# Kernel optimization log

Hardware: AMD Instinct MI355X
Metric: run time of the kernel (lower is better)

## Reference

```python
import jax, jax.numpy as jnp
import numpy as np


def setup_inputs() -> dict:
    key = jax.random.key(0)
    T, B, D, H = 512, 64, 512, 512
    k0, k1, k2, k3 = jax.random.split(key, 4)
    x = jax.random.normal(k0, (T, B, D), dtype=jnp.float32)
    # packed-sequence lengths, descending (as PackedSequence requires), at least T//2
    lengths = jnp.sort(jax.random.randint(k1, (B,), T // 2, T + 1))[::-1].astype(jnp.int64)
    s = 1.0 / np.sqrt(H)
    # gates stacked in order (i, f, c, o): same math as 8 separate per-gate linears
    Wx = jax.random.normal(k2, (4 * H, D), dtype=jnp.float32) * s
    Wh = jax.random.normal(k3, (4 * H, H), dtype=jnp.float32) * s
    # reset_parameters(): b_i = b_c = b_o = 0, b_f = 1
    b = jnp.concatenate([jnp.zeros(H), jnp.ones(H), jnp.zeros(2 * H)]).astype(jnp.float32)
    return {"x": x, "lengths": lengths, "Wx": Wx, "Wh": Wh, "b": b}


def reference(x, lengths, Wx, Wh, b):
    T, B, D = x.shape
    H = Wh.shape[1]
    # input projections for all timesteps at once (one big GEMM)
    xg = jnp.einsum('tbd,gd->tbg', x, Wx) + b  # [T, B, 4H]
    # validity mask per (t, b): packed recurrence only updates active rows
    mask = (jnp.arange(T)[:, None] < lengths[None, :])[..., None]  # [T, B, 1]

    def step(carry, inp):
        h, c = carry
        xg_t, m = inp
        g = xg_t + h @ Wh.T  # [B, 4H]
        i, f, cc, o = jnp.split(g, 4, axis=-1)
        i = jax.nn.sigmoid(i)
        f = jax.nn.sigmoid(f)
        o = jax.nn.sigmoid(o)
        c_t = f * c + i * jnp.tanh(cc)
        h_t = o * jnp.tanh(c_t)
        c_new = jnp.where(m, c_t, c)
        h_new = jnp.where(m, h_t, h)
        out_t = jnp.where(m, h_new, jnp.zeros((), x.dtype))
        return (h_new, c_new), out_t

    h0 = jnp.zeros((B, H), dtype=x.dtype)
    (h_T, c_T), out = jax.lax.scan(step, (h0, h0), (xg, mask))
    return out  # padded equivalent of the PackedSequence output, [T, B, H]
```

## Files before the change

kernel.cpp:

```cpp
#include <hip/hip_runtime.h>
#include <stdint.h>


#define TT 512
#define BB 64
#define DD 512
#define HH 512
#define NWG 256
#define NTHR 512
#define GR 8

typedef short short8 __attribute__((ext_vector_type(8)));
typedef float f32x4 __attribute__((ext_vector_type(4)));

__device__ __forceinline__ uint16_t bf16_rne(float f) {
  uint32_t u = __float_as_uint(f);
  u += 0x7fffu + ((u >> 16) & 1u);
  return (uint16_t)(u >> 16);
}

__device__ __forceinline__ void split2(float f, uint16_t &hi, uint16_t &lo) {
  uint16_t h = bf16_rne(f);
  hi = h;
  lo = bf16_rne(f - __uint_as_float(((uint32_t)h) << 16));
}

__device__ __forceinline__ float sigf(float v) { return 1.0f / (1.0f + __expf(-v)); }
__device__ __forceinline__ float tanh_(float v) {
  return 1.0f - 2.0f / (__expf(2.0f * v) + 1.0f);
}

__global__ void build_frags(const float* __restrict__ W, uint32_t* __restrict__ frag) {
  const int tid = blockIdx.x * 256 + threadIdx.x;
  const int lane = tid & 63;
  const int ks = (tid >> 6) & 15;
  const int nblk = tid >> 10;
  const int col = nblk * 16 + (lane & 15);
  const int k0 = ks * 32 + ((lane >> 4) << 3);
  const float* src = W + (size_t)col * 512 + k0;
  float4 a = *(const float4*)(src);
  float4 b = *(const float4*)(src + 4);
  float v[8] = {a.x, a.y, a.z, a.w, b.x, b.y, b.z, b.w};
  uint32_t hw[4], lw[4];
#pragma unroll
  for (int j = 0; j < 4; ++j) {
    uint16_t h0, l0, h1, l1;
    split2(v[2 * j], h0, l0);
    split2(v[2 * j + 1], h1, l1);
    hw[j] = (uint32_t)h0 | ((uint32_t)h1 << 16);
    lw[j] = (uint32_t)l0 | ((uint32_t)l1 << 16);
  }
  uint4* dst = (uint4*)(frag + (size_t)tid * 8);
  dst[0] = make_uint4(hw[0], hw[1], hw[2], hw[3]);
  dst[1] = make_uint4(lw[0], lw[1], lw[2], lw[3]);
}

__global__ __launch_bounds__(NTHR, 2) void lstm_main(
    const float* __restrict__ x, const int* __restrict__ len,
    const float* __restrict__ bias, const uint32_t* __restrict__ fragWx,
    const uint32_t* __restrict__ fragWh, uint32_t* __restrict__ h_pair,
    float* __restrict__ out) {
  const int tid = threadIdx.x;
  const int lane = tid & 63;
  const int wave = tid >> 6;
  const int gp = wave >> 1;
  const int kh = wave & 1;
  const int group = blockIdx.x & 7;
  const int jblk = blockIdx.x >> 3;
  const int b0 = group * GR;
  const int j0 = jblk << 4;
  uint32_t* hbase = h_pair + (size_t)group * 2 * (GR * HH);

  __shared__ uint16_t AH[GR * 512];
  __shared__ uint16_t AL[GR * 512];
  __shared__ float ex[8][GR][16];
  __shared__ float c_st[GR][16];
  __shared__ float h_st[GR][16];
  __shared__ float bias_l[4][16];
  __shared__ int len_l[GR];

  if (tid < GR * 16) {
    c_st[tid >> 4][tid & 15] = 0.0f;
    h_st[tid >> 4][tid & 15] = 0.0f;
  }
  if (tid < 64) bias_l[tid >> 4][tid & 15] = bias[(size_t)(tid >> 4) * HH + j0 + (tid & 15)];
  if (tid < GR) len_l[tid] = len[b0 + tid];

  short8 bxh[8], bxl[8], bhh[8], bhl[8];
  {
    const int nblk = gp * 32 + jblk;
#pragma unroll
    for (int ksl = 0; ksl < 8; ++ksl) {
      const size_t idx = ((size_t)(nblk * 16 + kh * 8 + ksl) * 64 + lane) * 8;
      uint4 vh = *(const uint4*)(fragWx + idx);
      uint4 vl = *(const uint4*)(fragWx + idx + 4);
      bxh[ksl] = __builtin_bit_cast(short8, vh);
      bxl[ksl] = __builtin_bit_cast(short8, vl);
      uint4 wh = *(const uint4*)(fragWh + idx);
      uint4 wl = *(const uint4*)(fragWh + idx + 4);
      bhh[ksl] = __builtin_bit_cast(short8, wh);
      bhl[ksl] = __builtin_bit_cast(short8, wl);
    }
  }

  const int arow = lane & 7;
  const int achk = (lane >> 4) << 4;
  const int axr = arow << 4;
  const char* rowH = (const char*)AH + arow * 1024;
  const char* rowL = (const char*)AL + arow * 1024;

  f32x4 hh = {0.f, 0.f, 0.f, 0.f}, lh = {0.f, 0.f, 0.f, 0.f}, hl = {0.f, 0.f, 0.f, 0.f};
  float4 xp[2];

#define LOAD_XP(tt)                                                            \
  _Pragma("unroll") for (int i = 0; i < 2; ++i) {                              \
    const int flat4 = i * 2048 + tid * 4;                                      \
    const int row = flat4 >> 9;                                                \
    const int col = flat4 & 511;                                               \
    xp[i] = *(const float4*)(x + ((size_t)(tt) * BB + b0 + row) * DD + col);   \
  }

#define STAGE_XP()                                                             \
  _Pragma("unroll") for (int i = 0; i < 2; ++i) {                              \
    const int flat4 = i * 2048 + tid * 4;                                      \
    const int row = flat4 >> 9;                                                \
    const int col = flat4 & 511;                                               \
    uint16_t h0, l0, h1, l1, h2, l2, h3, l3;                                   \
    split2(xp[i].x, h0, l0);                                                   \
    split2(xp[i].y, h1, l1);                                                   \
    split2(xp[i].z, h2, l2);                                                   \
    split2(xp[i].w, h3, l3);                                                   \
    const uint32_t hw0 = (uint32_t)h0 | ((uint32_t)h1 << 16);                  \
    const uint32_t hw1 = (uint32_t)h2 | ((uint32_t)h3 << 16);                  \
    const uint32_t lw0 = (uint32_t)l0 | ((uint32_t)l1 << 16);                  \
    const uint32_t lw1 = (uint32_t)l2 | ((uint32_t)l3 << 16);                  \
    const int off = row * 1024 + ((col * 2) ^ (row << 4));                     \
    *(uint2*)((char*)AH + off) = make_uint2(hw0, hw1);                         \
    *(uint2*)((char*)AL + off) = make_uint2(lw0, lw1);                         \
  }

#define X_MFMA()                                                               \
  hh = (f32x4){0.f, 0.f, 0.f, 0.f};                                           \
  lh = (f32x4){0.f, 0.f, 0.f, 0.f};                                           \
  hl = (f32x4){0.f, 0.f, 0.f, 0.f};                                           \
  _Pragma("unroll") for (int ksl = 0; ksl < 8; ++ksl) {                        \
    const int off = ((kh * 8 + ksl) * 64 + achk) ^ axr;                        \
    short8 ah = *(const short8*)(rowH + off);                                  \
    short8 al = *(const short8*)(rowL + off);                                  \
    hh = __builtin_amdgcn_mfma_f32_16x16x32_bf16(ah, bxh[ksl], hh, 0, 0, 0);   \
    lh = __builtin_amdgcn_mfma_f32_16x16x32_bf16(al, bxh[ksl], lh, 0, 0, 0);   \
    hl = __builtin_amdgcn_mfma_f32_16x16x32_bf16(ah, bxl[ksl], hl, 0, 0, 0);   \
  }

  LOAD_XP(0);
  __syncthreads();
  STAGE_XP();
  __syncthreads();
  X_MFMA();
  LOAD_XP(1);

  for (int t = 0; t < TT; ++t) {
    const int rbuf = t & 1;
    const int wbuf = rbuf ^ 1;

    if (t > 0) {
      const uint32_t tagp = (((uint32_t)(t - 1)) >> 1) & 3u;
      const uint32_t EXd = ((tagp & 1u) << 14) | ((tagp >> 1) << 30);
      const uint64_t EX2 = ((uint64_t)EXd << 32) | EXd;
      const uint64_t MK2 = 0x4000400040004000ull;
      const unsigned long long* pb =
          (const unsigned long long*)(hbase + (size_t)rbuf * (GR * HH)) +
          (size_t)tid * 4;
      uint64_t w0, w1, w2, w3;
      for (;;) {
        w0 = __hip_atomic_load(pb + 0, __ATOMIC_RELAXED, __HIP_MEMORY_SCOPE_AGENT);
        w1 = __hip_atomic_load(pb + 1, __ATOMIC_RELAXED, __HIP_MEMORY_SCOPE_AGENT);
        w2 = __hip_atomic_load(pb + 2, __ATOMIC_RELAXED, __HIP_MEMORY_SCOPE_AGENT);
        w3 = __hip_atomic_load(pb + 3, __ATOMIC_RELAXED, __HIP_MEMORY_SCOPE_AGENT);
        const uint64_t bad =
            (((w0 ^ EX2) | (w1 ^ EX2) | (w2 ^ EX2) | (w3 ^ EX2)) & MK2);
        if (bad == 0ull) break;
      }
      __syncthreads();

      {
        const uint32_t CM = ~0x40004000u;
        uint32_t d0 = (uint32_t)w0 & CM, d1 = (uint32_t)(w0 >> 32) & CM;
        uint32_t d2 = (uint32_t)w1 & CM, d3 = (uint32_t)(w1 >> 32) & CM;
        uint32_t d4 = (uint32_t)w2 & CM, d5 = (uint32_t)(w2 >> 32) & CM;
        uint32_t d6 = (uint32_t)w3 & CM, d7 = (uint32_t)(w3 >> 32) & CM;
        const uint32_t hi0 = (d0 & 0xFFFFu) | (d1 << 16);
        const uint32_t lo0 = (d0 >> 16) | (d1 & 0xFFFF0000u);
        const uint32_t hi1 = (d2 & 0xFFFFu) | (d3 << 16);
        const uint32_t lo1 = (d2 >> 16) | (d3 & 0xFFFF0000u);
        const uint32_t hi2 = (d4 & 0xFFFFu) | (d5 << 16);
        const uint32_t lo2 = (d4 >> 16) | (d5 & 0xFFFF0000u);
        const uint32_t hi3 = (d6 & 0xFFFFu) | (d7 << 16);
        const uint32_t lo3 = (d6 >> 16) | (d7 & 0xFFFF0000u);
        const int woff = wave * 1024 + ((lane * 16) ^ (wave << 4));
        *(uint4*)((char*)AH + woff) = make_uint4(hi0, hi1, hi2, hi3);
        *(uint4*)((char*)AL + woff) = make_uint4(lo0, lo1, lo2, lo3);
      }
      __syncthreads();

#pragma unroll
      for (int ksl = 0; ksl < 8; ++ksl) {
        const int off = ((kh * 8 + ksl) * 64 + achk) ^ axr;
        short8 ah = *(const short8*)(rowH + off);
        short8 al = *(const short8*)(rowL + off);
        hh = __builtin_amdgcn_mfma_f32_16x16x32_bf16(ah, bhh[ksl], hh, 0, 0, 0);
        lh = __builtin_amdgcn_mfma_f32_16x16x32_bf16(al, bhh[ksl], lh, 0, 0, 0);
        hl = __builtin_amdgcn_mfma_f32_16x16x32_bf16(ah, bhl[ksl], hl, 0, 0, 0);
      }
    }

    {
      const int crow = (lane >> 4) << 2;
      const int ccol = lane & 15;
      if (crow < GR) {
#pragma unroll
        for (int r = 0; r < 4; ++r) ex[wave][crow + r][ccol] = hh[r] + lh[r] + hl[r];
      }
    }
    __syncthreads();

    if (tid < GR * 16) {
      const int brow = tid >> 4;
      const int jc = tid & 15;
      const float p0 = ex[0][brow][jc] + ex[1][brow][jc] + bias_l[0][jc];
      const float p1 = ex[2][brow][jc] + ex[3][brow][jc] + bias_l[1][jc];
      const float p2 = ex[4][brow][jc] + ex[5][brow][jc] + bias_l[2][jc];
      const float p3 = ex[6][brow][jc] + ex[7][brow][jc] + bias_l[3][jc];
      const float ig = sigf(p0);
      const float fg = sigf(p1);
      const float cc = tanh_(p2);
      const float og = sigf(p3);
      const float co = c_st[brow][jc];
      const float ct = fg * co + ig * cc;
      const float ht = og * tanh_(ct);
      const bool m = (t < len_l[brow]);
      const float cn = m ? ct : co;
      const float hn = m ? ht : h_st[brow][jc];
      c_st[brow][jc] = cn;
      h_st[brow][jc] = hn;
      out[((size_t)t * BB + b0 + brow) * HH + j0 + jc] = m ? ht : 0.0f;
      uint16_t ph, pl;
      split2(hn, ph, pl);
      const uint32_t tagw = (((uint32_t)t) >> 1) & 3u;
      const uint32_t TB = ((tagw & 1u) << 14) | ((tagw >> 1) << 30);
      const uint32_t hv = ((uint32_t)ph | ((uint32_t)pl << 16)) | TB;
      __hip_atomic_store(hbase + (size_t)wbuf * (GR * HH) + brow * HH + j0 + jc,
                         hv, __ATOMIC_RELAXED, __HIP_MEMORY_SCOPE_AGENT);
    }

    if (t + 1 < TT) {
      STAGE_XP();
      __syncthreads();
      X_MFMA();
      LOAD_XP(min(t + 2, TT - 1));
    }
  }
}

extern "C" void kernel_launch(void* const* d_in, const int* in_sizes, int n_in,
                              void* d_out, int out_size, void* d_ws, size_t ws_size,
                              hipStream_t stream) {
  const float* x = (const float*)d_in[0];
  const int* len = (const int*)d_in[1];
  const float* Wx = (const float*)d_in[2];
  const float* Wh = (const float*)d_in[3];
  const float* bias = (const float*)d_in[4];
  float* out = (float*)d_out;

  const size_t FRAG_DW = (size_t)128 * 16 * 64 * 8;
  uint32_t* fragWx = (uint32_t*)d_ws;
  uint32_t* fragWh = fragWx + FRAG_DW;
  uint32_t* h_pair = fragWh + FRAG_DW;

  hipMemsetAsync(h_pair, 0xFF, (size_t)8 * 2 * GR * HH * 4, stream);

  build_frags<<<dim3(512), dim3(256), 0, stream>>>(Wx, fragWx);
  build_frags<<<dim3(512), dim3(256), 0, stream>>>(Wh, fragWh);

  void* args[] = {(void*)&x,      (void*)&len,    (void*)&bias, (void*)&fragWx,
                  (void*)&fragWh, (void*)&h_pair, (void*)&out};
  hipLaunchCooperativeKernel((void*)lstm_main, dim3(NWG), dim3(NTHR), args, 0, stream);
}
```

Baseline: 1.445 ms.

## Halve workgroups by doubling batch rows per group in the LSTM recurrence

Changes the work split from 8 batch groups of 8 rows to 4 groups of 16 rows, so 128 workgroups each fill the full 16-row MFMA tile instead of wasting half of it. Each thread now polls and unpacks 8 tagged h words, spinning on the first word before reading the rest, and the shared-memory swizzle is adjusted for 16 rows. Fewer workgroups take part in each step's cross-workgroup exchange, but each does twice the gate math and handles twice the x staging per step, which may lengthen the per-step critical path.

```diff
diff --git a/kernel.cpp b/kernel.cpp
--- a/kernel.cpp
+++ b/kernel.cpp
@@ -6,9 +6,9 @@
 #define BB 64
 #define DD 512
 #define HH 512
-#define NWG 256
+#define NWG 128
 #define NTHR 512
-#define GR 8
+#define GR 16
 
 typedef short short8 __attribute__((ext_vector_type(8)));
 typedef float f32x4 __attribute__((ext_vector_type(4)));
@@ -55,7 +55,7 @@
   dst[1] = make_uint4(lw[0], lw[1], lw[2], lw[3]);
 }
 
-__global__ __launch_bounds__(NTHR, 2) void lstm_main(
+__global__ __launch_bounds__(NTHR, 2) void lstm5(
     const float* __restrict__ x, const int* __restrict__ len,
     const float* __restrict__ bias, const uint32_t* __restrict__ fragWx,
     const uint32_t* __restrict__ fragWh, uint32_t* __restrict__ h_pair,
@@ -65,8 +65,8 @@
   const int wave = tid >> 6;
   const int gp = wave >> 1;
   const int kh = wave & 1;
-  const int group = blockIdx.x & 7;
-  const int jblk = blockIdx.x >> 3;
+  const int group = blockIdx.x & 3;
+  const int jblk = blockIdx.x >> 2;
   const int b0 = group * GR;
   const int j0 = jblk << 4;
   uint32_t* hbase = h_pair + (size_t)group * 2 * (GR * HH);
@@ -92,28 +92,27 @@
 #pragma unroll
     for (int ksl = 0; ksl < 8; ++ksl) {
       const size_t idx = ((size_t)(nblk * 16 + kh * 8 + ksl) * 64 + lane) * 8;
-      uint4 vh = *(const uint4*)(fragWx + idx);
-      uint4 vl = *(const uint4*)(fragWx + idx + 4);
-      bxh[ksl] = __builtin_bit_cast(short8, vh);
-      bxl[ksl] = __builtin_bit_cast(short8, vl);
-      uint4 wh = *(const uint4*)(fragWh + idx);
-      uint4 wl = *(const uint4*)(fragWh + idx + 4);
-      bhh[ksl] = __builtin_bit_cast(short8, wh);
-      bhl[ksl] = __builtin_bit_cast(short8, wl);
-    }
-  }
-
-  const int arow = lane & 7;
+      bxh[ksl] = __builtin_bit_cast(short8, *(const uint4*)(fragWx + idx));
+      bxl[ksl] = __builtin_bit_cast(short8, *(const uint4*)(fragWx + idx + 4));
+      bhh[ksl] = __builtin_bit_cast(short8, *(const uint4*)(fragWh + idx));
+      bhl[ksl] = __builtin_bit_cast(short8, *(const uint4*)(fragWh + idx + 4));
+    }
+  }
+
+  const int arow = lane & 15;
   const int achk = (lane >> 4) << 4;
-  const int axr = arow << 4;
+  const int axr = (arow & 7) << 4;
   const char* rowH = (const char*)AH + arow * 1024;
   const char* rowL = (const char*)AL + arow * 1024;
 
   f32x4 hh = {0.f, 0.f, 0.f, 0.f}, lh = {0.f, 0.f, 0.f, 0.f}, hl = {0.f, 0.f, 0.f, 0.f};
-  float4 xp[2];
+  float4 xp[4];
+
+  const uint64_t MK2 = 0x4000400040004000ull;
+  const uint32_t CM = ~0x40004000u;
 
 #define LOAD_XP(tt)                                                            \
-  _Pragma("unroll") for (int i = 0; i < 2; ++i) {                              \
+  _Pragma("unroll") for (int i = 0; i < 4; ++i) {                              \
     const int flat4 = i * 2048 + tid * 4;                                      \
     const int row = flat4 >> 9;                                                \
     const int col = flat4 & 511;                                               \
@@ -121,7 +120,7 @@
   }
 
 #define STAGE_XP()                                                             \
-  _Pragma("unroll") for (int i = 0; i < 2; ++i) {                              \
+  _Pragma("unroll") for (int i = 0; i < 4; ++i) {                              \
     const int flat4 = i * 2048 + tid * 4;                                      \
     const int row = flat4 >> 9;                                                \
     const int col = flat4 & 511;                                               \
@@ -134,7 +133,7 @@
     const uint32_t hw1 = (uint32_t)h2 | ((uint32_t)h3 << 16);                  \
     const uint32_t lw0 = (uint32_t)l0 | ((uint32_t)l1 << 16);                  \
     const uint32_t lw1 = (uint32_t)l2 | ((uint32_t)l3 << 16);                  \
-    const int off = row * 1024 + ((col * 2) ^ (row << 4));                     \
+    const int off = row * 1024 + ((col * 2) ^ ((row & 7) << 4));               \
     *(uint2*)((char*)AH + off) = make_uint2(hw0, hw1);                         \
     *(uint2*)((char*)AL + off) = make_uint2(lw0, lw1);                         \
   }
@@ -164,42 +163,51 @@
     const int wbuf = rbuf ^ 1;
 
     if (t > 0) {
-      const uint32_t tagp = (((uint32_t)(t - 1)) >> 1) & 3u;
-      const uint32_t EXd = ((tagp & 1u) << 14) | ((tagp >> 1) << 30);
-      const uint64_t EX2 = ((uint64_t)EXd << 32) | EXd;
-      const uint64_t MK2 = 0x4000400040004000ull;
+      const uint32_t tg = (((uint32_t)(t - 1)) >> 1) & 3u;
+      const uint32_t Ed = ((tg & 1u) << 14) | ((tg >> 1) << 30);
+      const uint64_t EX2 = ((uint64_t)Ed << 32) | Ed;
       const unsigned long long* pb =
           (const unsigned long long*)(hbase + (size_t)rbuf * (GR * HH)) +
-          (size_t)tid * 4;
-      uint64_t w0, w1, w2, w3;
+          (size_t)tid * 8;
+      uint64_t w[8];
+      do {
+        w[0] = __hip_atomic_load(pb, __ATOMIC_RELAXED, __HIP_MEMORY_SCOPE_AGENT);
+      } while ((w[0] ^ EX2) & MK2);
+#pragma unroll
+      for (int q = 1; q < 8; ++q)
+        w[q] = __hip_atomic_load(pb + q, __ATOMIC_RELAXED, __HIP_MEMORY_SCOPE_AGENT);
       for (;;) {
-        w0 = __hip_atomic_load(pb + 0, __ATOMIC_RELAXED, __HIP_MEMORY_SCOPE_AGENT);
-        w1 = __hip_atomic_load(pb + 1, __ATOMIC_RELAXED, __HIP_MEMORY_SCOPE_AGENT);
-        w2 = __hip_atomic_load(pb + 2, __ATOMIC_RELAXED, __HIP_MEMORY_SCOPE_AGENT);
-        w3 = __hip_atomic_load(pb + 3, __ATOMIC_RELAXED, __HIP_MEMORY_SCOPE_AGENT);
-        const uint64_t bad =
-            (((w0 ^ EX2) | (w1 ^ EX2) | (w2 ^ EX2) | (w3 ^ EX2)) & MK2);
-        if (bad == 0ull) break;
+        uint64_t bad = 0;
+#pragma unroll
+        for (int q = 1; q < 8; ++q) bad |= (w[q] ^ EX2);
+        if ((bad & MK2) == 0ull) break;
+#pragma unroll
+        for (int q = 1; q < 8; ++q)
+          w[q] = __hip_atomic_load(pb + q, __ATOMIC_RELAXED, __HIP_MEMORY_SCOPE_AGENT);
       }
       __syncthreads();
 
       {
-        const uint32_t CM = ~0x40004000u;
-        uint32_t d0 = (uint32_t)w0 & CM, d1 = (uint32_t)(w0 >> 32) & CM;
-        uint32_t d2 = (uint32_t)w1 & CM, d3 = (uint32_t)(w1 >> 32) & CM;
-        uint32_t d4 = (uint32_t)w2 & CM, d5 = (uint32_t)(w2 >> 32) & CM;
-        uint32_t d6 = (uint32_t)w3 & CM, d7 = (uint32_t)(w3 >> 32) & CM;
-        const uint32_t hi0 = (d0 & 0xFFFFu) | (d1 << 16);
-        const uint32_t lo0 = (d0 >> 16) | (d1 & 0xFFFF0000u);
-        const uint32_t hi1 = (d2 & 0xFFFFu) | (d3 << 16);
-        const uint32_t lo1 = (d2 >> 16) | (d3 & 0xFFFF0000u);
-        const uint32_t hi2 = (d4 & 0xFFFFu) | (d5 << 16);
-        const uint32_t lo2 = (d4 >> 16) | (d5 & 0xFFFF0000u);
-        const uint32_t hi3 = (d6 & 0xFFFFu) | (d7 << 16);
-        const uint32_t lo3 = (d6 >> 16) | (d7 & 0xFFFF0000u);
-        const int woff = wave * 1024 + ((lane * 16) ^ (wave << 4));
-        *(uint4*)((char*)AH + woff) = make_uint4(hi0, hi1, hi2, hi3);
-        *(uint4*)((char*)AL + woff) = make_uint4(lo0, lo1, lo2, lo3);
+        uint32_t d[16];
+#pragma unroll
+        for (int q = 0; q < 8; ++q) {
+          d[2 * q] = (uint32_t)w[q] & CM;
+          d[2 * q + 1] = (uint32_t)(w[q] >> 32) & CM;
+        }
+        uint32_t hw[8], lw[8];
+#pragma unroll
+        for (int j = 0; j < 8; ++j) {
+          hw[j] = (d[2 * j] & 0xFFFFu) | (d[2 * j + 1] << 16);
+          lw[j] = (d[2 * j] >> 16) | (d[2 * j + 1] & 0xFFFF0000u);
+        }
+        const int rrow = tid >> 5;
+        const int base = rrow * 1024;
+        const int swz = (rrow & 7) << 4;
+        const int cb = (tid & 31) * 32;
+        *(uint4*)((char*)AH + base + (cb ^ swz)) = make_uint4(hw[0], hw[1], hw[2], hw[3]);
+        *(uint4*)((char*)AH + base + ((cb + 16) ^ swz)) = make_uint4(hw[4], hw[5], hw[6], hw[7]);
+        *(uint4*)((char*)AL + base + (cb ^ swz)) = make_uint4(lw[0], lw[1], lw[2], lw[3]);
+        *(uint4*)((char*)AL + base + ((cb + 16) ^ swz)) = make_uint4(lw[4], lw[5], lw[6], lw[7]);
       }
       __syncthreads();
 
@@ -217,14 +225,12 @@
     {
       const int crow = (lane >> 4) << 2;
       const int ccol = lane & 15;
-      if (crow < GR) {
-#pragma unroll
-        for (int r = 0; r < 4; ++r) ex[wave][crow + r][ccol] = hh[r] + lh[r] + hl[r];
-      }
+#pragma unroll
+      for (int r = 0; r < 4; ++r) ex[wave][crow + r][ccol] = hh[r] + lh[r] + hl[r];
     }
     __syncthreads();
 
-    if (tid < GR * 16) {
+    if (tid < 256) {
       const int brow = tid >> 4;
       const int jc = tid & 15;
       const float p0 = ex[0][brow][jc] + ex[1][brow][jc] + bias_l[0][jc];
@@ -248,9 +254,9 @@
       split2(hn, ph, pl);
       const uint32_t tagw = (((uint32_t)t) >> 1) & 3u;
       const uint32_t TB = ((tagw & 1u) << 14) | ((tagw >> 1) << 30);
-      const uint32_t hv = ((uint32_t)ph | ((uint32_t)pl << 16)) | TB;
       __hip_atomic_store(hbase + (size_t)wbuf * (GR * HH) + brow * HH + j0 + jc,
-                         hv, __ATOMIC_RELAXED, __HIP_MEMORY_SCOPE_AGENT);
+                         ((uint32_t)ph | ((uint32_t)pl << 16)) | TB,
+                         __ATOMIC_RELAXED, __HIP_MEMORY_SCOPE_AGENT);
     }
 
     if (t + 1 < TT) {
@@ -260,6 +266,9 @@
       LOAD_XP(min(t + 2, TT - 1));
     }
   }
+#undef LOAD_XP
+#undef STAGE_XP
+#undef X_MFMA
 }
 
 extern "C" void kernel_launch(void* const* d_in, const int* in_sizes, int n_in,
@@ -273,16 +282,17 @@
   float* out = (float*)d_out;
 
   const size_t FRAG_DW = (size_t)128 * 16 * 64 * 8;
+  const size_t HP_DW = (size_t)4 * 2 * GR * HH;
   uint32_t* fragWx = (uint32_t*)d_ws;
   uint32_t* fragWh = fragWx + FRAG_DW;
   uint32_t* h_pair = fragWh + FRAG_DW;
 
-  hipMemsetAsync(h_pair, 0xFF, (size_t)8 * 2 * GR * HH * 4, stream);
+  hipMemsetAsync(h_pair, 0xFF, HP_DW * 4, stream);
 
   build_frags<<<dim3(512), dim3(256), 0, stream>>>(Wx, fragWx);
   build_frags<<<dim3(512), dim3(256), 0, stream>>>(Wh, fragWh);
 
   void* args[] = {(void*)&x,      (void*)&len,    (void*)&bias, (void*)&fragWx,
                   (void*)&fragWh, (void*)&h_pair, (void*)&out};
-  hipLaunchCooperativeKernel((void*)lstm_main, dim3(NWG), dim3(NTHR), args, 0, stream);
-}
+  hipLaunchCooperativeKernel((void*)lstm5, dim3(NWG), dim3(NTHR), args, 0, stream);
+}
```

After: 1.972 ms. 36.4% more time.
